# Performance work log

Measured on AMD Instinct MI355X. Metric: run time of the kernel, lower is better.

## Reference

```python
import jax, jax.numpy as jnp
import numpy as np

B, N, C, H, L, D_FF = 32, 196, 768, 12, 4, 3072

def _ln(x, g, b, eps=1e-6):
    m = x.mean(-1, keepdims=True)
    v = ((x - m) ** 2).mean(-1, keepdims=True)
    return (x - m) / jnp.sqrt(v + eps) * g + b

def _sdpa(q, k, v, scale):
    a = jax.nn.softmax(jnp.einsum('...qd,...kd->...qk', q, k) * scale, axis=-1)
    return jnp.einsum('...qk,...kd->...qd', a, v)

def _vit_attn(x, qkv_w, qkv_b, proj_w, proj_b):
    Bs, Ns, Cs = x.shape
    hd = Cs // H
    qkv = (x @ qkv_w + qkv_b).reshape(Bs, Ns, 3, H, hd).transpose(2, 0, 3, 1, 4)
    q, k, v = qkv[0], qkv[1], qkv[2]  # [B,H,N,hd]
    o = _sdpa(q, k, v, hd ** -0.5).transpose(0, 2, 1, 3).reshape(Bs, Ns, Cs)
    return o @ proj_w + proj_b

def _mlp(x, w1, b1, w2, b2):
    return jax.nn.gelu(x @ w1 + b1, approximate=False) @ w2 + b2

def setup_inputs() -> dict:
    key = jax.random.key(0)
    ks = jax.random.split(key, 16)
    w = lambda k, s: (jax.random.normal(k, s, jnp.float32) * 0.02)
    inp = {
        'x': jax.random.normal(ks[0], (B, N, C), jnp.float32),
        'y': jax.random.normal(ks[1], (B, N, C), jnp.float32),
        'latents': w(ks[2], (1, L, C)),
        'scale_a': jnp.zeros((1,), jnp.float32),
        'scale_v': jnp.zeros((1,), jnp.float32),
    }
    for i, p in enumerate(['s', 'r']):
        kk = jax.random.split(ks[3 + i], 4)
        inp.update({
            f'{p}_ln1_g': jnp.ones((C,), jnp.float32),
            f'{p}_ln1_b': jnp.zeros((C,), jnp.float32),
            f'{p}_qkv_w': w(kk[0], (C, 3 * C)),
            f'{p}_qkv_b': jnp.zeros((3 * C,), jnp.float32),
            f'{p}_proj_w': w(kk[1], (C, C)),
            f'{p}_proj_b': jnp.zeros((C,), jnp.float32),
            f'{p}_ln2_g': jnp.ones((C,), jnp.float32),
            f'{p}_ln2_b': jnp.zeros((C,), jnp.float32),
            f'{p}_fc1_w': w(kk[2], (C, D_FF)),
            f'{p}_fc1_b': jnp.zeros((D_FF,), jnp.float32),
            f'{p}_fc2_w': w(kk[3], (D_FF, C)),
            f'{p}_fc2_b': jnp.zeros((C,), jnp.float32),
        })
    return inp

def reference(x, y, latents, scale_a, scale_v,
              s_ln1_g, s_ln1_b, s_qkv_w, s_qkv_b, s_proj_w, s_proj_b,
              s_ln2_g, s_ln2_b, s_fc1_w, s_fc1_b, s_fc2_w, s_fc2_b,
              r_ln1_g, r_ln1_b, r_qkv_w, r_qkv_b, r_proj_w, r_proj_b,
              r_ln2_g, r_ln2_b, r_fc1_w, r_fc1_b, r_fc2_w, r_fc2_b):
    BS = x.shape[0]
    Cf = x.shape[-1]
    # --- latent bottleneck fusion (single-head, scale = C**-0.5) ---
    concat = jnp.concatenate([x, y], axis=1)            # [B, Na+Nv, C]
    lat = jnp.broadcast_to(latents, (BS,) + latents.shape[1:])
    fused = _sdpa(lat, concat, concat, Cf ** -0.5)      # [B, L, C]
    x = x + scale_a * _sdpa(x, fused, fused, Cf ** -0.5)
    y = y + scale_v * _sdpa(y, fused, fused, Cf ** -0.5)
    # --- standard ViT blocks per stream ---
    x = x + _vit_attn(_ln(x, s_ln1_g, s_ln1_b), s_qkv_w, s_qkv_b, s_proj_w, s_proj_b)
    y = y + _vit_attn(_ln(y, r_ln1_g, r_ln1_b), r_qkv_w, r_qkv_b, r_proj_w, r_proj_b)
    x = x + _mlp(_ln(x, s_ln2_g, s_ln2_b), s_fc1_w, s_fc1_b, s_fc2_w, s_fc2_b)
    y = y + _mlp(_ln(y, r_ln2_g, r_ln2_b), r_fc1_w, r_fc1_b, r_fc2_w, r_fc2_b)
    return (x, y)
```

## Files before the change

### kernel.cpp

```cpp
#include <hip/hip_runtime.h>
#include <hip/hip_bf16.h>
#include <math.h>

constexpr int Bc   = 32;
constexpr int Nc   = 196;
constexpr int Cc   = 768;
constexpr int Hc   = 12;
constexpr int HDc  = 64;
constexpr int Lc   = 4;
constexpr int DFFc = 3072;
constexpr int NCAT = 2 * Nc;
constexpr int Mrows = Bc * Nc;
constexpr float SCALE_C = 0.03608439182435161f;
constexpr float SCALE_H = 0.125f;
constexpr float LOG2E   = 1.4426950408889634f;

typedef __attribute__((ext_vector_type(8))) short short8;
typedef __attribute__((ext_vector_type(4))) short s16x4;
typedef __attribute__((ext_vector_type(4))) float float4a;
typedef __attribute__((ext_vector_type(4))) _Float16 half4;

__device__ inline float gelu_exact(float v) {
    return 0.5f * v * (1.0f + erff(v * 0.7071067811865476f));
}

__device__ inline void store_val(float* p, float v) { *p = v; }
__device__ inline void store_val(__hip_bfloat16* p, float v) { *p = __float2bfloat16(v); }

__device__ inline void gload16(const void* g, void* l) {
    __builtin_amdgcn_global_load_lds(
        (const __attribute__((address_space(1))) void*)g,
        (__attribute__((address_space(3))) void*)l, 16, 0, 0);
}

__global__ __launch_bounds__(256) void lat_scores_ker(
    const float* __restrict__ x, const float* __restrict__ y,
    const float* __restrict__ lat, float* __restrict__ scores)
{
    int wglobal = blockIdx.x * 4 + (threadIdx.x >> 6);
    int lane = threadIdx.x & 63;
    int b = wglobal / NCAT, j = wglobal % NCAT;
    const float* row = (j < Nc) ? x + ((size_t)b * Nc + j) * Cc
                                : y + ((size_t)b * Nc + (j - Nc)) * Cc;
    float a0 = 0.f, a1 = 0.f, a2 = 0.f, a3 = 0.f;
    for (int c = lane; c < Cc; c += 64) {
        float rv = row[c];
        a0 += rv * lat[c];
        a1 += rv * lat[Cc + c];
        a2 += rv * lat[2 * Cc + c];
        a3 += rv * lat[3 * Cc + c];
    }
    #pragma unroll
    for (int o = 32; o; o >>= 1) {
        a0 += __shfl_xor(a0, o);
        a1 += __shfl_xor(a1, o);
        a2 += __shfl_xor(a2, o);
        a3 += __shfl_xor(a3, o);
    }
    if (lane == 0) {
        float* sb = scores + (size_t)b * Lc * NCAT + j;
        sb[0 * NCAT] = a0 * SCALE_C;
        sb[1 * NCAT] = a1 * SCALE_C;
        sb[2 * NCAT] = a2 * SCALE_C;
        sb[3 * NCAT] = a3 * SCALE_C;
    }
}

__global__ __launch_bounds__(256) void lat_softmax_ker(float* __restrict__ scores)
{
    int b = blockIdx.x;
    int w = threadIdx.x >> 6, lane = threadIdx.x & 63;
    float* row = scores + (size_t)b * Lc * NCAT + w * NCAT;
    float m = -INFINITY;
    for (int j = lane; j < NCAT; j += 64) m = fmaxf(m, row[j]);
    #pragma unroll
    for (int o = 32; o; o >>= 1) m = fmaxf(m, __shfl_xor(m, o));
    float sum = 0.f;
    float e0 = expf(row[lane] - m);
    float e1 = expf(row[lane + 64] - m);
    float e2 = expf(row[lane + 128] - m);
    float e3 = expf(row[lane + 192] - m);
    float e4 = expf(row[lane + 256] - m);
    float e5 = expf(row[lane + 320] - m);
    float e6 = (lane < 8) ? expf(row[lane + 384] - m) : 0.f;
    sum = e0 + e1 + e2 + e3 + e4 + e5 + e6;
    #pragma unroll
    for (int o = 32; o; o >>= 1) sum += __shfl_xor(sum, o);
    float inv = 1.f / sum;
    row[lane] = e0 * inv;
    row[lane + 64] = e1 * inv;
    row[lane + 128] = e2 * inv;
    row[lane + 192] = e3 * inv;
    row[lane + 256] = e4 * inv;
    row[lane + 320] = e5 * inv;
    if (lane < 8) row[lane + 384] = e6 * inv;
}

__global__ __launch_bounds__(256) void lat_fused_ker(
    const float* __restrict__ x, const float* __restrict__ y,
    const float* __restrict__ probs, float* __restrict__ fused)
{
    int b = blockIdx.x, chunk = blockIdx.y;
    int t = threadIdx.x;
    int l = t >> 6;
    int c = chunk * 64 + (t & 63);
    __shared__ float p[Lc][NCAT];
    for (int idx = t; idx < Lc * NCAT; idx += 256)
        (&p[0][0])[idx] = probs[(size_t)b * Lc * NCAT + idx];
    __syncthreads();

    float acc0 = 0.f, acc1 = 0.f;
    for (int j = 0; j < Nc; j += 2) {
        const float* r0 = x + ((size_t)b * Nc + j) * Cc;
        acc0 += p[l][j] * r0[c];
        acc1 += p[l][j + 1] * r0[Cc + c];
    }
    for (int j = 0; j < Nc; j += 2) {
        const float* r0 = y + ((size_t)b * Nc + j) * Cc;
        acc0 += p[l][Nc + j] * r0[c];
        acc1 += p[l][Nc + j + 1] * r0[Cc + c];
    }
    fused[(size_t)b * Lc * Cc + l * Cc + c] = acc0 + acc1;
}

__global__ __launch_bounds__(256) void inject_ker(
    const float* __restrict__ x, const float* __restrict__ y,
    const float* __restrict__ fused,
    const float* __restrict__ scale_a, const float* __restrict__ scale_v,
    float* __restrict__ out)
{
    int gid = blockIdx.x;
    int st = gid / Mrows;
    int bn = gid % Mrows;
    int b = bn / Nc;
    const float* src = st ? y : x;
    float scale = st ? scale_v[0] : scale_a[0];
    float* dst = out + (size_t)st * Mrows * Cc;
    const float* f = fused + (size_t)b * Lc * Cc;
    const float* row = src + (size_t)bn * Cc;

    __shared__ float sc[4];
    int w = threadIdx.x >> 6, lane = threadIdx.x & 63;
    float partial = 0.f;
    for (int c = lane; c < Cc; c += 64) partial += row[c] * f[w * Cc + c];
    #pragma unroll
    for (int o = 32; o; o >>= 1) partial += __shfl_xor(partial, o);
    if (lane == 0) sc[w] = partial * SCALE_C;
    __syncthreads();

    float s0 = sc[0], s1 = sc[1], s2 = sc[2], s3 = sc[3];
    float m = fmaxf(fmaxf(s0, s1), fmaxf(s2, s3));
    float e0 = expf(s0 - m), e1 = expf(s1 - m), e2 = expf(s2 - m), e3 = expf(s3 - m);
    float inv = 1.f / (e0 + e1 + e2 + e3);
    e0 *= inv; e1 *= inv; e2 *= inv; e3 *= inv;

    for (int c = threadIdx.x; c < Cc; c += 256) {
        float v = e0 * f[c] + e1 * f[Cc + c] + e2 * f[2 * Cc + c] + e3 * f[3 * Cc + c];
        dst[(size_t)bn * Cc + c] = row[c] + scale * v;
    }
}

__global__ __launch_bounds__(256) void ln_ker(
    const float* __restrict__ in, size_t inz,
    const float* __restrict__ g0, const float* __restrict__ b0,
    const float* __restrict__ g1, const float* __restrict__ b1,
    __hip_bfloat16* __restrict__ out, size_t outz)
{
    int z = blockIdx.z;
    const float* g = z ? g1 : g0;
    const float* bb = z ? b1 : b0;
    in += (size_t)z * inz; out += (size_t)z * outz;

    int row = blockIdx.x;
    __shared__ float buf[Cc];
    __shared__ float red[4];
    __shared__ float red2[4];
    const float* r = in + (size_t)row * Cc;
    int w = threadIdx.x >> 6, lane = threadIdx.x & 63;

    float s = 0.f;
    for (int c = threadIdx.x; c < Cc; c += 256) {
        float v = r[c];
        buf[c] = v;
        s += v;
    }
    #pragma unroll
    for (int o = 32; o; o >>= 1) s += __shfl_xor(s, o);
    if (lane == 0) red[w] = s;
    __syncthreads();
    float mean = (red[0] + red[1] + red[2] + red[3]) * (1.f / Cc);

    float vs = 0.f;
    for (int c = threadIdx.x; c < Cc; c += 256) {
        float d = buf[c] - mean;
        vs += d * d;
    }
    #pragma unroll
    for (int o = 32; o; o >>= 1) vs += __shfl_xor(vs, o);
    if (lane == 0) red2[w] = vs;
    __syncthreads();
    float var = (red2[0] + red2[1] + red2[2] + red2[3]) * (1.f / Cc);
    float inv = 1.f / sqrtf(var + 1e-6f);

    for (int c = threadIdx.x; c < Cc; c += 256)
        out[(size_t)row * Cc + c] =
            __float2bfloat16((buf[c] - mean) * inv * g[c] + bb[c]);
}

struct WArgs {
    const float* src[8];
    __hip_bfloat16* dst[8];
};

__global__ __launch_bounds__(256) void wcast_all_ker(WArgs wa)
{
    int z = blockIdx.z;
    int bx = blockIdx.x;
    int which, tile, K_, N_;
    if (bx < 1728)      { which = 0; tile = bx;        K_ = 768;  N_ = 2304; }
    else if (bx < 2304) { which = 1; tile = bx - 1728; K_ = 768;  N_ = 768;  }
    else if (bx < 4608) { which = 2; tile = bx - 2304; K_ = 768;  N_ = 3072; }
    else                { which = 3; tile = bx - 4608; K_ = 3072; N_ = 768;  }
    const float* W = wa.src[z * 4 + which];
    __hip_bfloat16* WT = wa.dst[z * 4 + which];
    int ntx = N_ >> 5;
    int n0 = (tile % ntx) * 32, k0 = (tile / ntx) * 32;

    __shared__ float tilebuf[32][33];
    int t = threadIdx.x;
    int r = t >> 5, c = t & 31;
    #pragma unroll
    for (int p = 0; p < 4; ++p)
        tilebuf[r + p * 8][c] = W[(size_t)(k0 + r + p * 8) * N_ + n0 + c];
    __syncthreads();
    #pragma unroll
    for (int p = 0; p < 4; ++p)
        WT[(size_t)(n0 + r + p * 8) * K_ + k0 + c] =
            __float2bfloat16(tilebuf[c][r + p * 8]);
}

template <int EPI, typename OutT>
__global__ __launch_bounds__(256, 2) void gemm_bf16_ker(
    const __hip_bfloat16* __restrict__ A, size_t Az,
    const __hip_bfloat16* __restrict__ BT, size_t BTz,
    const float* __restrict__ bias0, const float* __restrict__ bias1,
    const float* __restrict__ res, size_t resz,
    OutT* __restrict__ out, size_t outz,
    int M_, int N_, int K_)
{
    const int z = blockIdx.z;
    A += (size_t)z * Az;
    BT += (size_t)z * BTz;
    const float* bias = z ? bias1 : bias0;
    res += (size_t)z * resz;
    out += (size_t)z * outz;

    __shared__ short As[128 * 32];
    __shared__ short Bs[128 * 32];
    const int t = threadIdx.x;
    const int wid = t >> 6, lane = t & 63;
    const int row0 = blockIdx.y * 128, col0 = blockIdx.x * 128;
    const int wr = (wid >> 1) * 64, wc = (wid & 1) * 64;

    const int f0 = wid * 1024 + lane * 16;
    const int f1 = f0 + 4096;
    const int r0s = f0 >> 6, r1s = f1 >> 6;
    const int u0 = ((f0 >> 4) & 3) ^ ((r0s >> 1) & 3);
    const int u1 = ((f1 >> 4) & 3) ^ ((r1s >> 1) & 3);

    const __hip_bfloat16* aS0 = A + (size_t)(row0 + r0s) * K_ + u0 * 8;
    const __hip_bfloat16* aS1 = A + (size_t)(row0 + r1s) * K_ + u1 * 8;
    const __hip_bfloat16* bS0 = BT + (size_t)(col0 + r0s) * K_ + u0 * 8;
    const __hip_bfloat16* bS1 = BT + (size_t)(col0 + r1s) * K_ + u1 * 8;
    short* ldsA0 = As + (wid * 1024) / 2;
    short* ldsA1 = As + (4096 + wid * 1024) / 2;
    short* ldsB0 = Bs + (wid * 1024) / 2;
    short* ldsB1 = Bs + (4096 + wid * 1024) / 2;

    const int fr = lane & 15;
    const int ku = lane >> 4;

    float4a acc[4][4];
    #pragma unroll
    for (int m = 0; m < 4; ++m)
        #pragma unroll
        for (int n = 0; n < 4; ++n)
            acc[m][n] = (float4a)0.f;

    for (int kt = 0; kt < K_; kt += 32) {
        gload16(aS0 + kt, ldsA0);
        gload16(aS1 + kt, ldsA1);
        gload16(bS0 + kt, ldsB0);
        gload16(bS1 + kt, ldsB1);
        __syncthreads();

        short8 af[4], bf[4];
        #pragma unroll
        for (int m = 0; m < 4; ++m) {
            int rl = wr + m * 16 + fr;
            int swz = ku ^ ((rl >> 1) & 3);
            af[m] = *(const short8*)(As + rl * 32 + swz * 8);
        }
        #pragma unroll
        for (int n = 0; n < 4; ++n) {
            int cl = wc + n * 16 + fr;
            int swz = ku ^ ((cl >> 1) & 3);
            bf[n] = *(const short8*)(Bs + cl * 32 + swz * 8);
        }
        #pragma unroll
        for (int m = 0; m < 4; ++m)
            #pragma unroll
            for (int n = 0; n < 4; ++n)
                acc[m][n] = __builtin_amdgcn_mfma_f32_16x16x32_bf16(
                    af[m], bf[n], acc[m][n], 0, 0, 0);
        __syncthreads();
    }

    const int fq = lane >> 4;
    #pragma unroll
    for (int m = 0; m < 4; ++m) {
        #pragma unroll
        for (int n = 0; n < 4; ++n) {
            int col = col0 + wc + n * 16 + fr;
            float b = bias[col];
            #pragma unroll
            for (int j = 0; j < 4; ++j) {
                int row = row0 + wr + m * 16 + fq * 4 + j;
                float v = acc[m][n][j] + b;
                if (EPI == 1) v = gelu_exact(v);
                if (EPI == 2) v += res[(size_t)row * N_ + col];
                store_val(out + (size_t)row * N_ + col, v);
            }
        }
    }
}

constexpr int NKT = 13;
constexpr int NQT = 13;
constexpr int NPAD = NKT * 16;
constexpr int VTS = 216;

__global__ __launch_bounds__(256) void attn_mfma_ker(
    const __hip_bfloat16* __restrict__ qkv, size_t qz,
    __hip_bfloat16* __restrict__ o, size_t oz)
{
    int z = blockIdx.z;
    qkv += (size_t)z * qz;
    o += (size_t)z * oz;

    int h = blockIdx.x, b = blockIdx.y;
    __shared__ short Ks[NPAD * 64];
    __shared__ _Float16 VT[64 * VTS];
    const size_t rs = 3 * Cc;
    const __hip_bfloat16* base = qkv + (size_t)b * Nc * rs + h * HDc;
    const int t = threadIdx.x;

    for (int c = t; c < NPAD * 8; c += 256) {
        int row = c >> 3, u = c & 7;
        int srow = row < Nc ? row : Nc - 1;
        short8 kv = *(const short8*)(base + (size_t)srow * rs + Cc + u * 8);
        *(short8*)(Ks + row * 64 + ((u ^ (row & 7)) << 3)) = kv;
        short8 vv = *(const short8*)(base + (size_t)srow * rs + 2 * Cc + u * 8);
        #pragma unroll
        for (int w = 0; w < 8; ++w) {
            __hip_bfloat16 bv = ((const __hip_bfloat16*)&vv)[w];
            VT[(u * 8 + w) * VTS + row] = (_Float16)__bfloat162float(bv);
        }
    }
    __syncthreads();

    const int wv = t >> 6, lane = t & 63;
    const int g = lane >> 4, c16 = lane & 15;
    const float KS = SCALE_H * LOG2E;

    for (int qt = wv; qt < NQT; qt += 4) {
        int qrow = qt * 16 + c16;
        int sq = qrow < Nc ? qrow : Nc - 1;
        const __hip_bfloat16* qb = base + (size_t)sq * rs + g * 8;
        short8 bq0 = *(const short8*)(qb);
        short8 bq1 = *(const short8*)(qb + 32);

        float4a acc[NKT];
        #pragma unroll
        for (int kt = 0; kt < NKT; ++kt) acc[kt] = (float4a)0.f;
        #pragma unroll
        for (int kt = 0; kt < NKT; ++kt) {
            int r = kt * 16 + c16;
            short8 a0 = *(const short8*)(Ks + r * 64 + ((g ^ (r & 7)) << 3));
            short8 a1 = *(const short8*)(Ks + r * 64 + (((4 + g) ^ (r & 7)) << 3));
            acc[kt] = __builtin_amdgcn_mfma_f32_16x16x32_bf16(a0, bq0, acc[kt], 0, 0, 0);
            acc[kt] = __builtin_amdgcn_mfma_f32_16x16x32_bf16(a1, bq1, acc[kt], 0, 0, 0);
        }

        float m = -INFINITY;
        #pragma unroll
        for (int kt = 0; kt < NKT; ++kt) {
            #pragma unroll
            for (int j = 0; j < 4; ++j) {
                int key = kt * 16 + g * 4 + j;
                float v = (key < Nc) ? acc[kt][j] * KS : -INFINITY;
                acc[kt][j] = v;
                m = fmaxf(m, v);
            }
        }
        m = fmaxf(m, __shfl_xor(m, 16));
        m = fmaxf(m, __shfl_xor(m, 32));

        float sum = 0.f;
        half4 pb[NKT];
        #pragma unroll
        for (int kt = 0; kt < NKT; ++kt) {
            #pragma unroll
            for (int j = 0; j < 4; ++j) {
                float e = exp2f(acc[kt][j] - m);
                sum += e;
                pb[kt][j] = (_Float16)e;
            }
        }
        sum += __shfl_xor(sum, 16);
        sum += __shfl_xor(sum, 32);
        float inv = 1.f / sum;

        float4a oa[4];
        #pragma unroll
        for (int dt = 0; dt < 4; ++dt) oa[dt] = (float4a)0.f;
        #pragma unroll
        for (int kt = 0; kt < NKT; ++kt) {
            #pragma unroll
            for (int dt = 0; dt < 4; ++dt) {
                half4 av = *(const half4*)(VT + (size_t)(dt * 16 + c16) * VTS
                                              + kt * 16 + g * 4);
                oa[dt] = __builtin_amdgcn_mfma_f32_16x16x16f16(av, pb[kt], oa[dt], 0, 0, 0);
            }
        }

        if (qrow < Nc) {
            __hip_bfloat16* ob = o + ((size_t)b * Nc + qrow) * Cc + h * HDc;
            #pragma unroll
            for (int dt = 0; dt < 4; ++dt) {
                __hip_bfloat16 tmp[4];
                #pragma unroll
                for (int j = 0; j < 4; ++j)
                    tmp[j] = __float2bfloat16(oa[dt][j] * inv);
                *(s16x4*)(ob + dt * 16 + g * 4) = *(const s16x4*)tmp;
            }
        }
    }
}

extern "C" void kernel_launch(void* const* d_in, const int* in_sizes, int n_in,
                              void* d_out, int out_size, void* d_ws, size_t ws_size,
                              hipStream_t stream)
{
    const float* x       = (const float*)d_in[0];
    const float* y       = (const float*)d_in[1];
    const float* latents = (const float*)d_in[2];
    const float* scale_a = (const float*)d_in[3];
    const float* scale_v = (const float*)d_in[4];

    float* out = (float*)d_out;

    constexpr size_t WSTREAM = 7077888;
    constexpr size_t OFF_QKV = 0;
    constexpr size_t OFF_PROJ = 2304 * 768;
    constexpr size_t OFF_FC1 = OFF_PROJ + 768 * 768;
    constexpr size_t OFF_FC2 = OFF_FC1 + 3072 * 768;

    constexpr size_t FRONT = ((size_t)Bc * Lc * NCAT + (size_t)Bc * Lc * Cc) * 4;
    constexpr size_t NEED_BATCH = FRONT
        + 2 * (size_t)Mrows * Cc * 2
        + 2 * (size_t)Mrows * DFFc * 2
        + 2 * WSTREAM * 2;

    float* ws = (float*)d_ws;
    float* scores = ws;
    float* fusedb = scores + (size_t)Bc * Lc * NCAT;

    const bool batched = ws_size >= NEED_BATCH;

    __hip_bfloat16* tbuf = (__hip_bfloat16*)(fusedb + (size_t)Bc * Lc * Cc);
    __hip_bfloat16* big;
    __hip_bfloat16* wT;
    if (batched) {
        big = tbuf + 2 * (size_t)Mrows * Cc;
        wT  = big + 2 * (size_t)Mrows * DFFc;
    } else {
        big = tbuf + (size_t)Mrows * Cc;
        wT  = big + (size_t)Mrows * DFFc;
    }

    lat_scores_ker<<<Bc * NCAT / 4, 256, 0, stream>>>(x, y, latents, scores);
    lat_softmax_ker<<<Bc, 256, 0, stream>>>(scores);
    lat_fused_ker<<<dim3(Bc, 12), 256, 0, stream>>>(x, y, scores, fusedb);
    inject_ker<<<2 * Mrows, 256, 0, stream>>>(x, y, fusedb, scale_a, scale_v, out);

    WArgs wa;
    for (int p = 0; p < 2; ++p) {
        int basei = 5 + 12 * p;
        wa.src[p * 4 + 0] = (const float*)d_in[basei + 2];
        wa.src[p * 4 + 1] = (const float*)d_in[basei + 4];
        wa.src[p * 4 + 2] = (const float*)d_in[basei + 8];
        wa.src[p * 4 + 3] = (const float*)d_in[basei + 10];
        wa.dst[p * 4 + 0] = wT + p * WSTREAM + OFF_QKV;
        wa.dst[p * 4 + 1] = wT + p * WSTREAM + OFF_PROJ;
        wa.dst[p * 4 + 2] = wT + p * WSTREAM + OFF_FC1;
        wa.dst[p * 4 + 3] = wT + p * WSTREAM + OFF_FC2;
    }
    wcast_all_ker<<<dim3(6912, 1, 2), 256, 0, stream>>>(wa);

    const float* g1[2], *b1[2], *qkvb[2], *projb[2], *g2[2], *b2[2], *fc1b[2], *fc2b[2];
    for (int p = 0; p < 2; ++p) {
        int basei = 5 + 12 * p;
        g1[p]    = (const float*)d_in[basei + 0];
        b1[p]    = (const float*)d_in[basei + 1];
        qkvb[p]  = (const float*)d_in[basei + 3];
        projb[p] = (const float*)d_in[basei + 5];
        g2[p]    = (const float*)d_in[basei + 6];
        b2[p]    = (const float*)d_in[basei + 7];
        fc1b[p]  = (const float*)d_in[basei + 9];
        fc2b[p]  = (const float*)d_in[basei + 11];
    }

    const size_t MC = (size_t)Mrows * Cc;
    const size_t MQKV = (size_t)Mrows * 2304;
    const size_t MFF = (size_t)Mrows * DFFc;

    if (batched) {
        ln_ker<<<dim3(Mrows, 1, 2), 256, 0, stream>>>(
            out, MC, g1[0], b1[0], g1[1], b1[1], tbuf, MC);
        gemm_bf16_ker<0, __hip_bfloat16><<<dim3(18, 49, 2), 256, 0, stream>>>(
            tbuf, MC, wT + OFF_QKV, WSTREAM, qkvb[0], qkvb[1],
            (const float*)out, 0, big, MQKV, Mrows, 2304, 768);
        attn_mfma_ker<<<dim3(Hc, Bc, 2), 256, 0, stream>>>(big, MQKV, tbuf, MC);
        gemm_bf16_ker<2, float><<<dim3(6, 49, 2), 256, 0, stream>>>(
            tbuf, MC, wT + OFF_PROJ, WSTREAM, projb[0], projb[1],
            (const float*)out, MC, out, MC, Mrows, 768, 768);
        ln_ker<<<dim3(Mrows, 1, 2), 256, 0, stream>>>(
            out, MC, g2[0], b2[0], g2[1], b2[1], tbuf, MC);
        gemm_bf16_ker<1, __hip_bfloat16><<<dim3(24, 49, 2), 256, 0, stream>>>(
            tbuf, MC, wT + OFF_FC1, WSTREAM, fc1b[0], fc1b[1],
            (const float*)out, 0, big, MFF, Mrows, 3072, 768);
        gemm_bf16_ker<2, float><<<dim3(6, 49, 2), 256, 0, stream>>>(
            big, MFF, wT + OFF_FC2, WSTREAM, fc2b[0], fc2b[1],
            (const float*)out, MC, out, MC, Mrows, 768, 3072);
    } else {
        for (int p = 0; p < 2; ++p) {
            float* X = out + (size_t)p * MC;
            __hip_bfloat16* wb = wT + p * WSTREAM;
            ln_ker<<<dim3(Mrows, 1, 1), 256, 0, stream>>>(
                X, 0, g1[p], b1[p], g1[p], b1[p], tbuf, 0);
            gemm_bf16_ker<0, __hip_bfloat16><<<dim3(18, 49, 1), 256, 0, stream>>>(
                tbuf, 0, wb + OFF_QKV, 0, qkvb[p], qkvb[p],
                (const float*)X, 0, big, 0, Mrows, 2304, 768);
            attn_mfma_ker<<<dim3(Hc, Bc, 1), 256, 0, stream>>>(big, 0, tbuf, 0);
            gemm_bf16_ker<2, float><<<dim3(6, 49, 1), 256, 0, stream>>>(
                tbuf, 0, wb + OFF_PROJ, 0, projb[p], projb[p],
                (const float*)X, 0, X, 0, Mrows, 768, 768);
            ln_ker<<<dim3(Mrows, 1, 1), 256, 0, stream>>>(
                X, 0, g2[p], b2[p], g2[p], b2[p], tbuf, 0);
            gemm_bf16_ker<1, __hip_bfloat16><<<dim3(24, 49, 1), 256, 0, stream>>>(
                tbuf, 0, wb + OFF_FC1, 0, fc1b[p], fc1b[p],
                (const float*)X, 0, big, 0, Mrows, 3072, 768);
            gemm_bf16_ker<2, float><<<dim3(6, 49, 1), 256, 0, stream>>>(
                big, 0, wb + OFF_FC2, 0, fc2b[p], fc2b[p],
                (const float*)X, 0, X, 0, Mrows, 768, 3072);
        }
    }
}
```

Baseline: 491.8 us.

## Double-buffer GEMM LDS tiles with BK=64 and XCD-aware block remapping

The bf16 GEMM kernel now uses two LDS buffers with a K-tile of 64, so global loads for the next tile are issued before the MFMAs on the current tile. This hides load latency behind compute and halves the number of barriers per K. The LDS swizzle is widened to 8 chunks to match the 128-byte rows. Block indices are also remapped so consecutive tiles land on the same XCD, which should improve L2 reuse. LDS use grows to 64KB per block, which may cut occupancy below the declared two blocks per CU.

```diff
diff --git a/kernel.cpp b/kernel.cpp
--- a/kernel.cpp
+++ b/kernel.cpp
@@ -248,37 +248,50 @@
     OutT* __restrict__ out, size_t outz,
     int M_, int N_, int K_)
 {
-    const int z = blockIdx.z;
+    const int gx = gridDim.x, gy = gridDim.y;
+    const long T = (long)gx * gy * gridDim.z;
+    long iflat = blockIdx.x + (long)gx * (blockIdx.y + (long)gy * blockIdx.z);
+    long q = T >> 3, r = T & 7;
+    long xcd = iflat & 7, jj = iflat >> 3;
+    long tt = (xcd < r ? xcd * (q + 1) : r * (q + 1) + (xcd - r) * q) + jj;
+    const int bx = (int)(tt % gx);
+    const int by = (int)((tt / gx) % gy);
+    const int z  = (int)(tt / ((long)gx * gy));
+
     A += (size_t)z * Az;
     BT += (size_t)z * BTz;
     const float* bias = z ? bias1 : bias0;
     res += (size_t)z * resz;
     out += (size_t)z * outz;
 
-    __shared__ short As[128 * 32];
-    __shared__ short Bs[128 * 32];
+    __shared__ short As[2][128 * 64];
+    __shared__ short Bs[2][128 * 64];
     const int t = threadIdx.x;
     const int wid = t >> 6, lane = t & 63;
-    const int row0 = blockIdx.y * 128, col0 = blockIdx.x * 128;
+    const int row0 = by * 128, col0 = bx * 128;
     const int wr = (wid >> 1) * 64, wc = (wid & 1) * 64;
 
-    const int f0 = wid * 1024 + lane * 16;
-    const int f1 = f0 + 4096;
-    const int r0s = f0 >> 6, r1s = f1 >> 6;
-    const int u0 = ((f0 >> 4) & 3) ^ ((r0s >> 1) & 3);
-    const int u1 = ((f1 >> 4) & 3) ^ ((r1s >> 1) & 3);
-
-    const __hip_bfloat16* aS0 = A + (size_t)(row0 + r0s) * K_ + u0 * 8;
-    const __hip_bfloat16* aS1 = A + (size_t)(row0 + r1s) * K_ + u1 * 8;
-    const __hip_bfloat16* bS0 = BT + (size_t)(col0 + r0s) * K_ + u0 * 8;
-    const __hip_bfloat16* bS1 = BT + (size_t)(col0 + r1s) * K_ + u1 * 8;
-    short* ldsA0 = As + (wid * 1024) / 2;
-    short* ldsA1 = As + (4096 + wid * 1024) / 2;
-    short* ldsB0 = Bs + (wid * 1024) / 2;
-    short* ldsB1 = Bs + (4096 + wid * 1024) / 2;
+    const __hip_bfloat16* aSrc[4];
+    const __hip_bfloat16* bSrc[4];
+    int ldsOff[4];
+    #pragma unroll
+    for (int ii = 0; ii < 4; ++ii) {
+        int f = wid * 1024 + ii * 4096 + lane * 16;
+        int rw = f >> 7;
+        int us = ((f >> 4) & 7) ^ (rw & 7);
+        aSrc[ii] = A + (size_t)(row0 + rw) * K_ + us * 8;
+        bSrc[ii] = BT + (size_t)(col0 + rw) * K_ + us * 8;
+        ldsOff[ii] = (wid * 1024 + ii * 4096) >> 1;
+    }
 
     const int fr = lane & 15;
     const int ku = lane >> 4;
+    int rlA[4], rlB[4];
+    #pragma unroll
+    for (int m = 0; m < 4; ++m) {
+        rlA[m] = wr + m * 16 + fr;
+        rlB[m] = wc + m * 16 + fr;
+    }
 
     float4a acc[4][4];
     #pragma unroll
@@ -287,34 +300,51 @@
         for (int n = 0; n < 4; ++n)
             acc[m][n] = (float4a)0.f;
 
-    for (int kt = 0; kt < K_; kt += 32) {
-        gload16(aS0 + kt, ldsA0);
-        gload16(aS1 + kt, ldsA1);
-        gload16(bS0 + kt, ldsB0);
-        gload16(bS1 + kt, ldsB1);
-        __syncthreads();
-
-        short8 af[4], bf[4];
-        #pragma unroll
-        for (int m = 0; m < 4; ++m) {
-            int rl = wr + m * 16 + fr;
-            int swz = ku ^ ((rl >> 1) & 3);
-            af[m] = *(const short8*)(As + rl * 32 + swz * 8);
-        }
-        #pragma unroll
-        for (int n = 0; n < 4; ++n) {
-            int cl = wc + n * 16 + fr;
-            int swz = ku ^ ((cl >> 1) & 3);
-            bf[n] = *(const short8*)(Bs + cl * 32 + swz * 8);
-        }
-        #pragma unroll
-        for (int m = 0; m < 4; ++m)
-            #pragma unroll
-            for (int n = 0; n < 4; ++n)
-                acc[m][n] = __builtin_amdgcn_mfma_f32_16x16x32_bf16(
-                    af[m], bf[n], acc[m][n], 0, 0, 0);
-        __syncthreads();
-    }
+#define STAGE(BUFSEL, KT)                                                   \
+    {                                                                       \
+        _Pragma("unroll")                                                   \
+        for (int ii = 0; ii < 4; ++ii) {                                    \
+            gload16(aSrc[ii] + (KT) * 64, &As[BUFSEL][ldsOff[ii]]);         \
+            gload16(bSrc[ii] + (KT) * 64, &Bs[BUFSEL][ldsOff[ii]]);         \
+        }                                                                   \
+    }
+
+    const int NT = K_ >> 6;
+    STAGE(0, 0);
+    asm volatile("s_waitcnt vmcnt(0)" ::: "memory");
+    __builtin_amdgcn_s_barrier();
+
+    int cur = 0;
+    for (int kt = 0; kt < NT; ++kt) {
+        if (kt + 1 < NT) STAGE(cur ^ 1, kt + 1);
+
+        const short* Ab = &As[cur][0];
+        const short* Bb = &Bs[cur][0];
+        #pragma unroll
+        for (int s = 0; s < 2; ++s) {
+            short8 af[4], bf8[4];
+            #pragma unroll
+            for (int m = 0; m < 4; ++m) {
+                int u = (s * 4 + ku) ^ (rlA[m] & 7);
+                af[m] = *(const short8*)(Ab + rlA[m] * 64 + u * 8);
+            }
+            #pragma unroll
+            for (int n = 0; n < 4; ++n) {
+                int u = (s * 4 + ku) ^ (rlB[n] & 7);
+                bf8[n] = *(const short8*)(Bb + rlB[n] * 64 + u * 8);
+            }
+            #pragma unroll
+            for (int m = 0; m < 4; ++m)
+                #pragma unroll
+                for (int n = 0; n < 4; ++n)
+                    acc[m][n] = __builtin_amdgcn_mfma_f32_16x16x32_bf16(
+                        af[m], bf8[n], acc[m][n], 0, 0, 0);
+        }
+        asm volatile("s_waitcnt vmcnt(0)" ::: "memory");
+        __builtin_amdgcn_s_barrier();
+        cur ^= 1;
+    }
+#undef STAGE
 
     const int fq = lane >> 4;
     #pragma unroll
```

Result: slower. 505.1 us (+2.7%).
